# Performance work log

Measured on AMD Instinct MI355X. Metric: run time of the kernel, lower is better.

Reference implementation:

```python
import jax, jax.numpy as jnp
import numpy as np
import math

D_MODEL = 1024
N_HEADS = 16
HEAD_DIM = D_MODEL // N_HEADS  # 64
N_FEATURES = 256
EPS = 1e-06


def _make_orthogonal_features(seed=0):
    # Blocks of QR-orthogonalized gaussian matrices, scaled by sqrt(head_dim)
    rng = np.random.default_rng(seed)
    n_blocks = math.ceil(N_FEATURES / HEAD_DIM)
    blocks = []
    for _ in range(n_blocks):
        q, _ = np.linalg.qr(rng.standard_normal((HEAD_DIM, HEAD_DIM)))
        blocks.append(q)
    mat = np.concatenate(blocks, axis=0)[:N_FEATURES] * math.sqrt(HEAD_DIM)
    return jnp.asarray(mat, dtype=jnp.float32)  # [M, head_dim]


def setup_inputs() -> dict:
    key = jax.random.key(0)
    ks = jax.random.split(key, 6)
    B, L = 4, 4096
    x = jax.random.normal(ks[0], (B, L, D_MODEL), dtype=jnp.float32)

    def lin(k):
        W = jax.random.normal(k, (D_MODEL, D_MODEL), dtype=jnp.float32) * 0.02
        b = jnp.zeros((D_MODEL,), dtype=jnp.float32)
        return W, b

    Wq, bq = lin(ks[1])
    Wk, bk = lin(ks[2])
    Wv, bv = lin(ks[3])
    Wo, bo = lin(ks[4])
    omega = _make_orthogonal_features(0)
    return {"x": x, "Wq": Wq, "bq": bq, "Wk": Wk, "bk": bk,
            "Wv": Wv, "bv": bv, "Wo": Wo, "bo": bo,
            "omega": omega, "causal": 1}


def _phi(x, omega):
    # positive random feature map: exp(omega^T xs - ||xs||^2/2) / sqrt(M)
    xs = x * (HEAD_DIM ** -0.25)                       # [B,H,L,D]
    x_omega = jnp.einsum('bhld,md->bhlm', xs, omega)   # [B,H,L,M]
    x_norm_sq = 0.5 * jnp.sum(xs * xs, axis=-1, keepdims=True)
    return jnp.exp(x_omega - x_norm_sq) / math.sqrt(N_FEATURES)


def _bidirectional(qp, kp, v):
    kv = jnp.einsum('bhlm,bhld->bhmd', kp, v)
    qkv = jnp.einsum('bhlm,bhmd->bhld', qp, kv)
    k_sum = jnp.sum(kp, axis=2)                        # [B,H,M]
    normalizer = jnp.einsum('bhlm,bhm->bhl', qp, k_sum)[..., None] + EPS
    return qkv / normalizer


def _causal(qp, kp, v):
    # prefix-sum recurrence over time via lax.scan
    qs = jnp.moveaxis(qp, 2, 0)   # [L,B,H,M]
    ks = jnp.moveaxis(kp, 2, 0)   # [L,B,H,M]
    vs = jnp.moveaxis(v, 2, 0)    # [L,B,H,D]
    B, H = v.shape[0], v.shape[1]
    kv0 = jnp.zeros((B, H, N_FEATURES, HEAD_DIM), dtype=v.dtype)
    ksum0 = jnp.zeros((B, H, N_FEATURES), dtype=v.dtype)

    def step(carry, inp):
        kv, ksum = carry
        q_t, k_t, v_t = inp
        kv = kv + k_t[..., :, None] * v_t[..., None, :]   # [B,H,M,D]
        ksum = ksum + k_t                                  # [B,H,M]
        num = jnp.einsum('bhm,bhmd->bhd', q_t, kv)
        den = jnp.einsum('bhm,bhm->bh', q_t, ksum)[..., None] + EPS
        return (kv, ksum), num / den

    _, out = jax.lax.scan(step, (kv0, ksum0), (qs, ks, vs))  # out: [L,B,H,D]
    return jnp.moveaxis(out, 0, 2)  # [B,H,L,D]


def reference(x, Wq, bq, Wk, bk, Wv, bv, Wo, bo, omega, causal):
    B, L, _ = x.shape

    def proj(W, b):
        return (x @ W + b).reshape(B, L, N_HEADS, HEAD_DIM).transpose(0, 2, 1, 3)

    q = proj(Wq, bq)
    k = proj(Wk, bk)
    v = proj(Wv, bv)
    qp = _phi(q, omega)
    kp = _phi(k, omega)
    if causal:
        out = _causal(qp, kp, v)
    else:
        out = _bidirectional(qp, kp, v)
    out = out.transpose(0, 2, 1, 3).reshape(B, L, D_MODEL)
    return out @ Wo + bo
```

## Files before the change

kernel.cpp:

```cpp
#include <hip/hip_runtime.h>
#include <hip/hip_bf16.h>


#define B_ 4
#define H_ 16
#define L_ 4096
#define D_ 64
#define M_ 256
#define DM_ 1024
#define BH_ 64
#define NSC 32

typedef unsigned int u32;
typedef unsigned short u16;
typedef __attribute__((ext_vector_type(8))) short bf16x8;
typedef __attribute__((ext_vector_type(4))) float f32x4;

static __device__ __forceinline__ float bf2f(u16 u) {
  return __uint_as_float(((u32)u) << 16);
}
static __device__ __forceinline__ u16 f2bf(float f) {
  u32 x = __float_as_uint(f);
  return (u16)((x + 0x7fffu + ((x >> 16) & 1u)) >> 16);
}
#define MFMA16(a, b, c) __builtin_amdgcn_mfma_f32_16x16x32_bf16((a), (b), (c), 0, 0, 0)

__global__ __launch_bounds__(256) void prep_k(
    const float* __restrict__ x, u16* __restrict__ xb,
    const float* __restrict__ W0, const float* __restrict__ W1,
    const float* __restrict__ W2, const float* __restrict__ W3,
    u16* __restrict__ Wt, const float* __restrict__ om,
    u16* __restrict__ omb) {
  __shared__ u16 tt[64][66];
  const int bid = blockIdx.x, tid = threadIdx.x;
  if (bid < 16384) {
    const int i = bid * 256 + tid;
    float4 f = ((const float4*)x)[i];
    ushort4 u;
    u.x = f2bf(f.x); u.y = f2bf(f.y); u.z = f2bf(f.z); u.w = f2bf(f.w);
    ((ushort4*)xb)[i] = u;
  } else if (bid < 17408) {
    const int rem = bid - 16384;
    const int z = rem >> 8, r2 = rem & 255;
    const int k0 = (r2 >> 4) * 64, n0 = (r2 & 15) * 64;
    const float* W = (z == 0) ? W0 : (z == 1) ? W1 : (z == 2) ? W2 : W3;
    u16* o = Wt + (size_t)z * 1048576ull;
    const int r = tid >> 4, c4 = (tid & 15) << 2;
    for (int rr = r; rr < 64; rr += 16) {
      float4 w4 = *(const float4*)(W + (size_t)(k0 + rr) * DM_ + n0 + c4);
      tt[c4 + 0][rr] = f2bf(w4.x);
      tt[c4 + 1][rr] = f2bf(w4.y);
      tt[c4 + 2][rr] = f2bf(w4.z);
      tt[c4 + 3][rr] = f2bf(w4.w);
    }
    __syncthreads();
    for (int rr = r; rr < 64; rr += 16) {
      ushort4 u4;
      u4.x = tt[rr][c4 + 0];
      u4.y = tt[rr][c4 + 1];
      u4.z = tt[rr][c4 + 2];
      u4.w = tt[rr][c4 + 3];
      *(ushort4*)(o + (size_t)(n0 + rr) * DM_ + k0 + c4) = u4;
    }
  } else {
    const int i = (bid - 17408) * 256 + tid;
    omb[i] = f2bf(om[i] * 0.35355339059327373f);
  }
}

__global__ __launch_bounds__(256) void mm3_k(
    const u16* __restrict__ A, const u16* __restrict__ Wt,
    const float* __restrict__ bq, const float* __restrict__ bk,
    const float* __restrict__ bv, u16* __restrict__ qb,
    u16* __restrict__ kb, u16* __restrict__ vb,
    float* __restrict__ nhq, float* __restrict__ nhk) {
  __shared__ u16 sA[128][64];
  __shared__ u16 sB[128][64];
  const int y = blockIdx.y;
  const u16* Bt = Wt + (size_t)y * 1048576ull;
  const float* bias = (y == 0) ? bq : (y == 1) ? bk : bv;
  u16* outp = (y == 0) ? qb : (y == 1) ? kb : vb;
  float* nhout = (y == 0) ? nhq : (y == 1) ? nhk : nullptr;
  const int tid = threadIdx.x, lane = tid & 63, w = tid >> 6;
  const int fr = lane & 15, fg = lane >> 4;
  const int wr = w >> 1, wc = w & 1;
  const int lb = ((blockIdx.x & 7) << 7) | (blockIdx.x >> 3);
  const int m0 = (lb >> 3) * 128, n0 = (lb & 7) * 128;
  const int srow = tid >> 3, sslot = tid & 7;
  f32x4 acc[4][4] = {};
  bf16x8 av[4], bv4[4];
#pragma unroll
  for (int p = 0; p < 4; ++p) {
    av[p]  = *(const bf16x8*)(A  + (size_t)(m0 + srow + p * 32) * DM_ + sslot * 8);
    bv4[p] = *(const bf16x8*)(Bt + (size_t)(n0 + srow + p * 32) * DM_ + sslot * 8);
  }
  for (int k0 = 0; k0 < DM_; k0 += 64) {
    __syncthreads();
#pragma unroll
    for (int p = 0; p < 4; ++p) {
      const int r = srow + p * 32;
      *(bf16x8*)&sA[r][(sslot ^ (r & 7)) * 8] = av[p];
      *(bf16x8*)&sB[r][(sslot ^ (r & 7)) * 8] = bv4[p];
    }
    if (k0 + 64 < DM_) {
#pragma unroll
      for (int p = 0; p < 4; ++p) {
        av[p]  = *(const bf16x8*)(A  + (size_t)(m0 + srow + p * 32) * DM_ + k0 + 64 + sslot * 8);
        bv4[p] = *(const bf16x8*)(Bt + (size_t)(n0 + srow + p * 32) * DM_ + k0 + 64 + sslot * 8);
      }
    }
    __syncthreads();
#pragma unroll
    for (int ks = 0; ks < 2; ++ks) {
      bf16x8 af[4], bf[4];
#pragma unroll
      for (int i = 0; i < 4; ++i) {
        const int r = wr * 64 + i * 16 + fr;
        af[i] = *(const bf16x8*)&sA[r][((ks * 4 + fg) ^ (r & 7)) * 8];
      }
#pragma unroll
      for (int j = 0; j < 4; ++j) {
        const int r = wc * 64 + j * 16 + fr;
        bf[j] = *(const bf16x8*)&sB[r][((ks * 4 + fg) ^ (r & 7)) * 8];
      }
#pragma unroll
      for (int i = 0; i < 4; ++i)
#pragma unroll
        for (int j = 0; j < 4; ++j)
          acc[i][j] = MFMA16(af[i], bf[j], acc[i][j]);
    }
  }
  const int m_blk = m0 + wr * 64, n_blk = n0 + wc * 64;
  float nhacc[4][4] = {};
#pragma unroll
  for (int j = 0; j < 4; ++j) {
    const int n = n_blk + j * 16 + fr;
    const float bi = bias[n];
    const int h = n >> 6, d = n & 63;
#pragma unroll
    for (int i = 0; i < 4; ++i) {
#pragma unroll
      for (int r = 0; r < 4; ++r) {
        const int m = m_blk + i * 16 + fg * 4 + r;
        const float val = acc[i][j][r] + bi;
        const int b = m >> 12, l = m & 4095;
        const u16 sv = f2bf(val);
        outp[((size_t)(b * H_ + h) * L_ + l) * D_ + d] = sv;
        const float rv = bf2f(sv);
        nhacc[i][r] += rv * rv;
      }
    }
  }
  if (nhout) {
    const int hh2 = n_blk >> 6;
#pragma unroll
    for (int i = 0; i < 4; ++i)
#pragma unroll
      for (int r = 0; r < 4; ++r) {
        float s = nhacc[i][r];
        s += __shfl_xor(s, 1, 64);
        s += __shfl_xor(s, 2, 64);
        s += __shfl_xor(s, 4, 64);
        s += __shfl_xor(s, 8, 64);
        if (fr == 0) {
          const int m = m_blk + i * 16 + fg * 4 + r;
          const int b = m >> 12, l = m & 4095;
          nhout[(size_t)(b * H_ + hh2) * L_ + l] = 0.0625f * s;
        }
      }
  }
}

__global__ __launch_bounds__(256) void mmo_k(
    const u16* __restrict__ A, const u16* __restrict__ Bt,
    const float* __restrict__ bias, float* __restrict__ outp) {
  __shared__ u16 sA[128][64];
  __shared__ u16 sB[128][64];
  const int tid = threadIdx.x, lane = tid & 63, w = tid >> 6;
  const int fr = lane & 15, fg = lane >> 4;
  const int wr = w >> 1, wc = w & 1;
  const int lb = ((blockIdx.x & 7) << 7) | (blockIdx.x >> 3);
  const int m0 = (lb >> 3) * 128, n0 = (lb & 7) * 128;
  const int srow = tid >> 3, sslot = tid & 7;
  f32x4 acc[4][4] = {};
  bf16x8 av[4], bv[4];
#pragma unroll
  for (int p = 0; p < 4; ++p) {
    av[p] = *(const bf16x8*)(A  + (size_t)(m0 + srow + p * 32) * DM_ + sslot * 8);
    bv[p] = *(const bf16x8*)(Bt + (size_t)(n0 + srow + p * 32) * DM_ + sslot * 8);
  }
  for (int k0 = 0; k0 < DM_; k0 += 64) {
    __syncthreads();
#pragma unroll
    for (int p = 0; p < 4; ++p) {
      const int r = srow + p * 32;
      *(bf16x8*)&sA[r][(sslot ^ (r & 7)) * 8] = av[p];
      *(bf16x8*)&sB[r][(sslot ^ (r & 7)) * 8] = bv[p];
    }
    if (k0 + 64 < DM_) {
#pragma unroll
      for (int p = 0; p < 4; ++p) {
        av[p] = *(const bf16x8*)(A  + (size_t)(m0 + srow + p * 32) * DM_ + k0 + 64 + sslot * 8);
        bv[p] = *(const bf16x8*)(Bt + (size_t)(n0 + srow + p * 32) * DM_ + k0 + 64 + sslot * 8);
      }
    }
    __syncthreads();
#pragma unroll
    for (int ks = 0; ks < 2; ++ks) {
      bf16x8 af[4], bf[4];
#pragma unroll
      for (int i = 0; i < 4; ++i) {
        const int r = wr * 64 + i * 16 + fr;
        af[i] = *(const bf16x8*)&sA[r][((ks * 4 + fg) ^ (r & 7)) * 8];
      }
#pragma unroll
      for (int j = 0; j < 4; ++j) {
        const int r = wc * 64 + j * 16 + fr;
        bf[j] = *(const bf16x8*)&sB[r][((ks * 4 + fg) ^ (r & 7)) * 8];
      }
#pragma unroll
      for (int i = 0; i < 4; ++i)
#pragma unroll
        for (int j = 0; j < 4; ++j)
          acc[i][j] = MFMA16(af[i], bf[j], acc[i][j]);
    }
  }
  const int m_blk = m0 + wr * 64, n_blk = n0 + wc * 64;
#pragma unroll
  for (int j = 0; j < 4; ++j) {
    const int n = n_blk + j * 16 + fr;
    const float bi = bias[n];
#pragma unroll
    for (int i = 0; i < 4; ++i)
#pragma unroll
      for (int r = 0; r < 4; ++r) {
        const int m = m_blk + i * 16 + fg * 4 + r;
        outp[(size_t)m * DM_ + n] = acc[i][j][r] + bi;
      }
  }
}

__global__ __launch_bounds__(256) void kvstate_k(
    const u16* __restrict__ k, const u16* __restrict__ v,
    const u16* __restrict__ omb, const float* __restrict__ nhk,
    u16* __restrict__ stateb, float* __restrict__ ksum) {
  __shared__ u16 sPhi[256][72];
  __shared__ u16 sVt[64][72];
  const int tid = threadIdx.x, lane = tid & 63, w = tid >> 6;
  const int fr = lane & 15, fg = lane >> 4;
  const int sc = blockIdx.x, bh = blockIdx.y;
  const size_t base_l = (size_t)bh * L_ + (size_t)sc * 128;

  bf16x8 ones;
#pragma unroll
  for (int e = 0; e < 8; ++e) ones[e] = (short)0x3F80;

  f32x4 kvacc[4][4] = {};
  f32x4 ksacc[4] = {};

  for (int sub = 0; sub < 2; ++sub) {
    const size_t tl = base_l + sub * 64;
    const u16* kg = k + tl * 64;
    __syncthreads();
    {
      const u16* vp = v + (tl + lane) * 64 + w * 16;
      bf16x8 v0 = *(const bf16x8*)(vp);
      bf16x8 v1 = *(const bf16x8*)(vp + 8);
#pragma unroll
      for (int e = 0; e < 8; ++e) sVt[w * 16 + e][lane] = (u16)v0[e];
#pragma unroll
      for (int e = 0; e < 8; ++e) sVt[w * 16 + 8 + e][lane] = (u16)v1[e];
    }
    float nhr[4];
#pragma unroll
    for (int tt = 0; tt < 4; ++tt) nhr[tt] = nhk[tl + tt * 16 + fr];
#pragma unroll
    for (int mi = 0; mi < 4; ++mi) {
      const int m0 = (w << 6) + mi * 16;
      const bf16x8 a0 = *(const bf16x8*)(omb + (m0 + fr) * 64 + fg * 8);
      const bf16x8 a1 = *(const bf16x8*)(omb + (m0 + fr) * 64 + 32 + fg * 8);
#pragma unroll
      for (int tt = 0; tt < 4; ++tt) {
        const bf16x8 b0 = *(const bf16x8*)(kg + (tt * 16 + fr) * 64 + fg * 8);
        const bf16x8 b1 = *(const bf16x8*)(kg + (tt * 16 + fr) * 64 + 32 + fg * 8);
        f32x4 acc = {0.f, 0.f, 0.f, 0.f};
        acc = MFMA16(a0, b0, acc);
        acc = MFMA16(a1, b1, acc);
        const float nhv = nhr[tt];
#pragma unroll
        for (int r = 0; r < 4; ++r)
          sPhi[m0 + fg * 4 + r][tt * 16 + fr] = f2bf(__expf(acc[r] - nhv) * 0.0625f);
      }
    }
    __syncthreads();
#pragma unroll
    for (int mi = 0; mi < 4; ++mi) {
      const int m0 = (w << 6) + mi * 16;
      const bf16x8 pb0 = *(const bf16x8*)&sPhi[m0 + fr][fg * 8];
      const bf16x8 pb1 = *(const bf16x8*)&sPhi[m0 + fr][32 + fg * 8];
      ksacc[mi] = MFMA16(pb0, ones, ksacc[mi]);
      ksacc[mi] = MFMA16(pb1, ones, ksacc[mi]);
#pragma unroll
      for (int dj = 0; dj < 4; ++dj) {
        const bf16x8 va0 = *(const bf16x8*)&sVt[dj * 16 + fr][fg * 8];
        const bf16x8 va1 = *(const bf16x8*)&sVt[dj * 16 + fr][32 + fg * 8];
        kvacc[mi][dj] = MFMA16(va0, pb0, kvacc[mi][dj]);
        kvacc[mi][dj] = MFMA16(va1, pb1, kvacc[mi][dj]);
      }
    }
  }
  u16* stb = stateb + (size_t)(bh * NSC + sc) * (M_ * D_);
  float* ksp = ksum + (size_t)(bh * NSC + sc) * M_;
#pragma unroll
  for (int mi = 0; mi < 4; ++mi) {
    const int m = (w << 6) + mi * 16 + fr;
#pragma unroll
    for (int dj = 0; dj < 4; ++dj)
#pragma unroll
      for (int r = 0; r < 4; ++r)
        stb[(size_t)(dj * 16 + fg * 4 + r) * M_ + m] = f2bf(kvacc[mi][dj][r]);
    if (fr == 0) {
#pragma unroll
      for (int r = 0; r < 4; ++r)
        ksp[(w << 6) + mi * 16 + fg * 4 + r] = ksacc[mi][r];
    }
  }
}

__global__ __launch_bounds__(256) void scan_k(u16* __restrict__ stateb,
                                              float* __restrict__ ksum) {
  const int bh = blockIdx.y;
  u16* sb = stateb + (size_t)bh * NSC * (M_ * D_);
  const int base = blockIdx.x * 2048 + threadIdx.x * 8;
  float run[8] = {};
  for (int cc = 0; cc < NSC; ++cc) {
    u16* st = sb + (size_t)cc * (M_ * D_) + base;
    ushort4 t0 = *(ushort4*)st;
    ushort4 t1 = *(ushort4*)(st + 4);
    ushort4 w0, w1;
    w0.x = f2bf(run[0]); w0.y = f2bf(run[1]); w0.z = f2bf(run[2]); w0.w = f2bf(run[3]);
    w1.x = f2bf(run[4]); w1.y = f2bf(run[5]); w1.z = f2bf(run[6]); w1.w = f2bf(run[7]);
    *(ushort4*)st = w0;
    *(ushort4*)(st + 4) = w1;
    run[0] += bf2f(t0.x); run[1] += bf2f(t0.y); run[2] += bf2f(t0.z); run[3] += bf2f(t0.w);
    run[4] += bf2f(t1.x); run[5] += bf2f(t1.y); run[6] += bf2f(t1.z); run[7] += bf2f(t1.w);
  }
  if (blockIdx.x == 0) {
    float rk = 0.f;
    for (int cc = 0; cc < NSC; ++cc) {
      float* p = ksum + (size_t)(bh * NSC + cc) * M_ + threadIdx.x;
      const float t = *p;
      *p = rk;
      rk += t;
    }
  }
}

static __device__ __forceinline__ void phi_quad(
    const u16* __restrict__ xg, const u16* __restrict__ ombq,
    u16* __restrict__ dst, int dstride, const float* nhv,
    int wb, int lane) {
  const int fr = lane & 15, fg = lane >> 4;
  const int tband = wb * 16;
  const bf16x8 a0 = *(const bf16x8*)(xg + (tband + fr) * 64 + fg * 8);
  const bf16x8 a1 = *(const bf16x8*)(xg + (tband + fr) * 64 + 32 + fg * 8);
#pragma unroll
  for (int j = 0; j < 4; ++j) {
    const bf16x8 b0 = *(const bf16x8*)(ombq + (j * 16 + fr) * 64 + fg * 8);
    const bf16x8 b1 = *(const bf16x8*)(ombq + (j * 16 + fr) * 64 + 32 + fg * 8);
    f32x4 acc = {0.f, 0.f, 0.f, 0.f};
    acc = MFMA16(a0, b0, acc);
    acc = MFMA16(a1, b1, acc);
#pragma unroll
    for (int r = 0; r < 4; ++r) {
      const int t = tband + fg * 4 + r;
      dst[t * dstride + j * 16 + fr] = f2bf(__expf(acc[r] - nhv[r]) * 0.0625f);
    }
  }
}

__global__ __launch_bounds__(512) void outchunk_k(
    const u16* __restrict__ q, const u16* __restrict__ kk,
    const u16* __restrict__ v, const u16* __restrict__ omb,
    const u16* __restrict__ stateb, const float* __restrict__ ksum,
    const float* __restrict__ nhq, const float* __restrict__ nhk,
    u16* __restrict__ attn) {
  __shared__ u16 sKa[64][264];
  __shared__ u16 sKb[64][264];
  __shared__ u16 sS0[64][72];
  __shared__ u16 sS1[64][72];
  __shared__ u16 sB1[64][72];
  __shared__ u16 sB2[64][72];
  __shared__ float ksum_l[256];
  const int tid = threadIdx.x, lane = tid & 63, w = tid >> 6;
  const int h = w >> 2, wl = w & 3;
  const int fr = lane & 15, fg = lane >> 4;
  const int bh = blockIdx.x >> 5, sc = blockIdx.x & 31;
  const size_t base_l = (size_t)bh * L_ + (size_t)sc * 128;
  const size_t tokq = base_l + (size_t)h * 64;
  const u16* qg = q + tokq * 64;
  const u16* stgb = stateb + (size_t)(bh * NSC + sc) * (M_ * D_);
  const float* ksg = ksum + (size_t)(bh * NSC + sc) * M_;

  if (tid < 256) ksum_l[tid] = ksg[tid];

  float nhq4[4];
#pragma unroll
  for (int r = 0; r < 4; ++r) nhq4[r] = nhq[tokq + wl * 16 + fg * 4 + r];

  u16* myscr = (h == 0) ? &sKa[0][0] : &sKb[0][0];
  bf16x8 qa0[2], qa1[2], qa2[2], qa3[2];
  f32x4 oacc[4] = {};
#define QPHASE(MQ, QA)                                                          \
  {                                                                             \
    bf16x8 b0r[4], b1r[4];                                                      \
    _Pragma("unroll")                                                           \
    for (int j = 0; j < 4; ++j) {                                               \
      b0r[j] = *(const bf16x8*)(stgb + (size_t)(j * 16 + fr) * M_ + MQ * 64 + fg * 8);        \
      b1r[j] = *(const bf16x8*)(stgb + (size_t)(j * 16 + fr) * M_ + MQ * 64 + 32 + fg * 8);   \
    }                                                                           \
    phi_quad(qg, omb + MQ * 4096, myscr, 264, nhq4, wl, lane);                  \
    QA[0] = *(const bf16x8*)(myscr + (wl * 16 + fr) * 264 + fg * 8);            \
    QA[1] = *(const bf16x8*)(myscr + (wl * 16 + fr) * 264 + 32 + fg * 8);       \
    __builtin_amdgcn_s_setprio(1);                                              \
    _Pragma("unroll")                                                           \
    for (int j = 0; j < 4; ++j) {                                               \
      oacc[j] = MFMA16(QA[0], b0r[j], oacc[j]);                                 \
      oacc[j] = MFMA16(QA[1], b1r[j], oacc[j]);                                 \
    }                                                                           \
    __builtin_amdgcn_s_setprio(0);                                              \
  }
  QPHASE(0, qa0)
  QPHASE(1, qa1)
  QPHASE(2, qa2)
  QPHASE(3, qa3)
#undef QPHASE
  __syncthreads();

  float denk = 0.f;
#pragma unroll
  for (int e = 0; e < 8; ++e) {
    denk += bf2f((u16)qa0[0][e]) * ksum_l[0   + fg * 8 + e]
          + bf2f((u16)qa0[1][e]) * ksum_l[32  + fg * 8 + e]
          + bf2f((u16)qa1[0][e]) * ksum_l[64  + fg * 8 + e]
          + bf2f((u16)qa1[1][e]) * ksum_l[96  + fg * 8 + e]
          + bf2f((u16)qa2[0][e]) * ksum_l[128 + fg * 8 + e]
          + bf2f((u16)qa2[1][e]) * ksum_l[160 + fg * 8 + e]
          + bf2f((u16)qa3[0][e]) * ksum_l[192 + fg * 8 + e]
          + bf2f((u16)qa3[1][e]) * ksum_l[224 + fg * 8 + e];
  }
  denk += __shfl_xor(denk, 16, 64);
  denk += __shfl_xor(denk, 32, 64);

  {
    const size_t ktokh = base_l + (size_t)h * 64;
    const u16* kgh = kk + ktokh * 64;
    float nhkh[4];
#pragma unroll
    for (int r = 0; r < 4; ++r) nhkh[r] = nhk[ktokh + wl * 16 + fg * 4 + r];
#pragma unroll
    for (int mq = 0; mq < 4; ++mq)
      phi_quad(kgh, omb + mq * 4096, myscr + mq * 64, 264, nhkh, wl, lane);
  }
  bf16x8 v0 = {}, v1 = {}, v2 = {}, v3 = {};
  if (h == 0) {
    const u16* vp0 = v + (base_l + lane) * 64 + wl * 16;
    const u16* vp1 = v + (base_l + 64 + lane) * 64 + wl * 16;
    v0 = *(const bf16x8*)(vp0);
    v1 = *(const bf16x8*)(vp0 + 8);
    v2 = *(const bf16x8*)(vp1);
    v3 = *(const bf16x8*)(vp1 + 8);
  }
  __syncthreads();

  float dS[4] = {0.f, 0.f, 0.f, 0.f};
  {
    f32x4 sacc[4] = {};
    __builtin_amdgcn_s_setprio(1);
#define SPH0(MQ, QA)                                                            \
    _Pragma("unroll")                                                           \
    for (int j = 0; j < 4; ++j) {                                               \
      const bf16x8 b0 = *(const bf16x8*)&sKa[j * 16 + fr][MQ * 64 + fg * 8];    \
      const bf16x8 b1 = *(const bf16x8*)&sKa[j * 16 + fr][MQ * 64 + 32 + fg * 8]; \
      sacc[j] = MFMA16(QA[0], b0, sacc[j]);                                     \
      sacc[j] = MFMA16(QA[1], b1, sacc[j]);                                     \
    }
    SPH0(0, qa0)
    SPH0(1, qa1)
    SPH0(2, qa2)
    SPH0(3, qa3)
#undef SPH0
    __builtin_amdgcn_s_setprio(0);
    u16 (*sSo)[72] = (h == 0) ? sS0 : sS1;
#pragma unroll
    for (int j = 0; j < 4; ++j)
#pragma unroll
      for (int r = 0; r < 4; ++r) {
        const int ss = j * 16 + fr, t = wl * 16 + fg * 4 + r;
        float val = sacc[j][r];
        if (h == 0 && ss > t) val = 0.f;
        const u16 vb = f2bf(val);
        sSo[t][ss] = vb;
        dS[r] += bf2f(vb);
      }
  }
  if (h == 0) {
#pragma unroll
    for (int e = 0; e < 8; ++e) sB1[wl * 16 + e][lane] = (u16)v0[e];
#pragma unroll
    for (int e = 0; e < 8; ++e) sB1[wl * 16 + 8 + e][lane] = (u16)v1[e];
#pragma unroll
    for (int e = 0; e < 8; ++e) sB2[wl * 16 + e][lane] = (u16)v2[e];
#pragma unroll
    for (int e = 0; e < 8; ++e) sB2[wl * 16 + 8 + e][lane] = (u16)v3[e];
  }
  __syncthreads();

  {
    const u16 (*sSo)[72] = (h == 0) ? sS0 : sS1;
    const bf16x8 a0 = *(const bf16x8*)&sSo[wl * 16 + fr][fg * 8];
    const bf16x8 a1 = *(const bf16x8*)&sSo[wl * 16 + fr][32 + fg * 8];
    __builtin_amdgcn_s_setprio(1);
#pragma unroll
    for (int j = 0; j < 4; ++j) {
      const bf16x8 b0 = *(const bf16x8*)&sB1[j * 16 + fr][fg * 8];
      const bf16x8 b1 = *(const bf16x8*)&sB1[j * 16 + fr][32 + fg * 8];
      oacc[j] = MFMA16(a0, b0, oacc[j]);
      oacc[j] = MFMA16(a1, b1, oacc[j]);
    }
    __builtin_amdgcn_s_setprio(0);
  }

  if (h == 1) {
    f32x4 sacc[4] = {};
    __builtin_amdgcn_s_setprio(1);
#define SPH1(MQ, QA)                                                            \
    _Pragma("unroll")                                                           \
    for (int j = 0; j < 4; ++j) {                                               \
      const bf16x8 b0 = *(const bf16x8*)&sKb[j * 16 + fr][MQ * 64 + fg * 8];    \
      const bf16x8 b1 = *(const bf16x8*)&sKb[j * 16 + fr][MQ * 64 + 32 + fg * 8]; \
      sacc[j] = MFMA16(QA[0], b0, sacc[j]);                                     \
      sacc[j] = MFMA16(QA[1], b1, sacc[j]);                                     \
    }
    SPH1(0, qa0)
    SPH1(1, qa1)
    SPH1(2, qa2)
    SPH1(3, qa3)
#undef SPH1
    __builtin_amdgcn_s_setprio(0);
#pragma unroll
    for (int j = 0; j < 4; ++j)
#pragma unroll
      for (int r = 0; r < 4; ++r) {
        const int ss = j * 16 + fr, t = wl * 16 + fg * 4 + r;
        float val = sacc[j][r];
        if (ss > t) val = 0.f;
        const u16 vb = f2bf(val);
        sS1[t][ss] = vb;
        dS[r] += bf2f(vb);
      }
    {
      const bf16x8 a0 = *(const bf16x8*)&sS1[wl * 16 + fr][fg * 8];
      const bf16x8 a1 = *(const bf16x8*)&sS1[wl * 16 + fr][32 + fg * 8];
      __builtin_amdgcn_s_setprio(1);
#pragma unroll
      for (int j = 0; j < 4; ++j) {
        const bf16x8 b0 = *(const bf16x8*)&sB2[j * 16 + fr][fg * 8];
        const bf16x8 b1 = *(const bf16x8*)&sB2[j * 16 + fr][32 + fg * 8];
        oacc[j] = MFMA16(a0, b0, oacc[j]);
        oacc[j] = MFMA16(a1, b1, oacc[j]);
      }
      __builtin_amdgcn_s_setprio(0);
    }
  }

#pragma unroll
  for (int m2 = 1; m2 <= 8; m2 <<= 1) {
#pragma unroll
    for (int r = 0; r < 4; ++r) dS[r] += __shfl_xor(dS[r], m2, 64);
  }
  const int b = bh >> 4, hh = bh & 15;
#pragma unroll
  for (int r = 0; r < 4; ++r) {
    const float dk = __shfl(denk, fg * 4 + r, 64);
    const float rinv = 1.0f / (dk + dS[r] + 1e-6f);
    const int t = wl * 16 + fg * 4 + r;
    const int l = sc * 128 + h * 64 + t;
#pragma unroll
    for (int j = 0; j < 4; ++j) {
      const int d = j * 16 + fr;
      attn[((size_t)b * L_ + l) * DM_ + hh * 64 + d] = f2bf(oacc[j][r] * rinv);
    }
  }
}

extern "C" void kernel_launch(void* const* d_in, const int* in_sizes, int n_in,
                              void* d_out, int out_size, void* d_ws, size_t ws_size,
                              hipStream_t stream) {
  const float* x     = (const float*)d_in[0];
  const float* Wq    = (const float*)d_in[1];
  const float* bq    = (const float*)d_in[2];
  const float* Wk    = (const float*)d_in[3];
  const float* bk    = (const float*)d_in[4];
  const float* Wv    = (const float*)d_in[5];
  const float* bv    = (const float*)d_in[6];
  const float* Wo    = (const float*)d_in[7];
  const float* bo    = (const float*)d_in[8];
  const float* omega = (const float*)d_in[9];
  float* out = (float*)d_out;

  char* ws = (char*)d_ws;
  u16*   v      = (u16*)(ws);
  u16*   qb     = (u16*)(ws + 33554432ull);
  u16*   kb     = (u16*)(ws + 67108864ull);
  u16*   xb     = (u16*)(ws + 100663296ull);
  u16*   attn   = xb;
  u16*   stateb = (u16*)(ws + 134217728ull);
  float* ksum   = (float*)(ws + 201326592ull);
  u16*   Wt     = (u16*)(ws + 203423744ull);
  u16*   omb    = (u16*)(ws + 211812352ull);
  float* nhq    = (float*)(ws + 211845120ull);
  float* nhk    = (float*)(ws + 212893696ull);

  prep_k<<<17472, 256, 0, stream>>>(x, xb, Wq, Wk, Wv, Wo, Wt, omega, omb);
  mm3_k<<<dim3(1024, 3), 256, 0, stream>>>(xb, Wt, bq, bk, bv,
                                           qb, kb, v, nhq, nhk);
  kvstate_k<<<dim3(NSC, BH_), 256, 0, stream>>>(kb, v, omb, nhk, stateb, ksum);
  scan_k<<<dim3(8, BH_), 256, 0, stream>>>(stateb, ksum);
  outchunk_k<<<BH_ * NSC, 512, 0, stream>>>(qb, kb, v, omb, stateb, ksum,
                                            nhq, nhk, attn);
  mmo_k<<<1024, 256, 0, stream>>>(attn, Wt + 3145728ull, bo, out);
}
```

Before: 516.2 us.

## Hoist key feature map before query phase and drop a block barrier

Computes the key feature map into shared memory before the query-phase work and moves the query scratch buffer to the S tiles, so one __syncthreads between the query phase and the S computation can be removed. V loads are split across both halves of the block, with each half transposing 64 tokens instead of one half doing all 128. This reduces barrier stalls and balances the V-transpose work. The query scratch now aliases sS0/sS1, which are later overwritten by S, so correctness depends on barrier ordering that has to be checked.

```diff
diff --git a/kernel.cpp b/kernel.cpp
--- a/kernel.cpp
+++ b/kernel.cpp
@@ -404,11 +404,29 @@
 
   if (tid < 256) ksum_l[tid] = ksg[tid];
 
+  bf16x8 ev0, ev1;
+  {
+    const u16* vp = v + (base_l + (size_t)h * 64 + lane) * 64 + wl * 16;
+    ev0 = *(const bf16x8*)(vp);
+    ev1 = *(const bf16x8*)(vp + 8);
+  }
+
+  u16* kdst = (h == 0) ? &sKa[0][0] : &sKb[0][0];
+  {
+    const size_t ktokh = base_l + (size_t)h * 64;
+    const u16* kgh = kk + ktokh * 64;
+    float nhkh[4];
+#pragma unroll
+    for (int r = 0; r < 4; ++r) nhkh[r] = nhk[ktokh + wl * 16 + fg * 4 + r];
+#pragma unroll
+    for (int mq = 0; mq < 4; ++mq)
+      phi_quad(kgh, omb + mq * 4096, kdst + mq * 64, 264, nhkh, wl, lane);
+  }
+
   float nhq4[4];
 #pragma unroll
   for (int r = 0; r < 4; ++r) nhq4[r] = nhq[tokq + wl * 16 + fg * 4 + r];
-
-  u16* myscr = (h == 0) ? &sKa[0][0] : &sKb[0][0];
+  u16* myscr = (h == 0) ? &sS0[0][0] : &sS1[0][0];
   bf16x8 qa0[2], qa1[2], qa2[2], qa3[2];
   f32x4 oacc[4] = {};
 #define QPHASE(MQ, QA)                                                          \
@@ -419,9 +437,9 @@
       b0r[j] = *(const bf16x8*)(stgb + (size_t)(j * 16 + fr) * M_ + MQ * 64 + fg * 8);        \
       b1r[j] = *(const bf16x8*)(stgb + (size_t)(j * 16 + fr) * M_ + MQ * 64 + 32 + fg * 8);   \
     }                                                                           \
-    phi_quad(qg, omb + MQ * 4096, myscr, 264, nhq4, wl, lane);                  \
-    QA[0] = *(const bf16x8*)(myscr + (wl * 16 + fr) * 264 + fg * 8);            \
-    QA[1] = *(const bf16x8*)(myscr + (wl * 16 + fr) * 264 + 32 + fg * 8);       \
+    phi_quad(qg, omb + MQ * 4096, myscr, 72, nhq4, wl, lane);                   \
+    QA[0] = *(const bf16x8*)(myscr + (wl * 16 + fr) * 72 + fg * 8);             \
+    QA[1] = *(const bf16x8*)(myscr + (wl * 16 + fr) * 72 + 32 + fg * 8);        \
     __builtin_amdgcn_s_setprio(1);                                              \
     _Pragma("unroll")                                                           \
     for (int j = 0; j < 4; ++j) {                                               \
@@ -451,27 +469,6 @@
   }
   denk += __shfl_xor(denk, 16, 64);
   denk += __shfl_xor(denk, 32, 64);
-
-  {
-    const size_t ktokh = base_l + (size_t)h * 64;
-    const u16* kgh = kk + ktokh * 64;
-    float nhkh[4];
-#pragma unroll
-    for (int r = 0; r < 4; ++r) nhkh[r] = nhk[ktokh + wl * 16 + fg * 4 + r];
-#pragma unroll
-    for (int mq = 0; mq < 4; ++mq)
-      phi_quad(kgh, omb + mq * 4096, myscr + mq * 64, 264, nhkh, wl, lane);
-  }
-  bf16x8 v0 = {}, v1 = {}, v2 = {}, v3 = {};
-  if (h == 0) {
-    const u16* vp0 = v + (base_l + lane) * 64 + wl * 16;
-    const u16* vp1 = v + (base_l + 64 + lane) * 64 + wl * 16;
-    v0 = *(const bf16x8*)(vp0);
-    v1 = *(const bf16x8*)(vp0 + 8);
-    v2 = *(const bf16x8*)(vp1);
-    v3 = *(const bf16x8*)(vp1 + 8);
-  }
-  __syncthreads();
 
   float dS[4] = {0.f, 0.f, 0.f, 0.f};
   {
@@ -504,15 +501,12 @@
         dS[r] += bf2f(vb);
       }
   }
-  if (h == 0) {
-#pragma unroll
-    for (int e = 0; e < 8; ++e) sB1[wl * 16 + e][lane] = (u16)v0[e];
-#pragma unroll
-    for (int e = 0; e < 8; ++e) sB1[wl * 16 + 8 + e][lane] = (u16)v1[e];
-#pragma unroll
-    for (int e = 0; e < 8; ++e) sB2[wl * 16 + e][lane] = (u16)v2[e];
-#pragma unroll
-    for (int e = 0; e < 8; ++e) sB2[wl * 16 + 8 + e][lane] = (u16)v3[e];
+  {
+    u16 (*sBo)[72] = (h == 0) ? sB1 : sB2;
+#pragma unroll
+    for (int e = 0; e < 8; ++e) sBo[wl * 16 + e][lane] = (u16)ev0[e];
+#pragma unroll
+    for (int e = 0; e < 8; ++e) sBo[wl * 16 + 8 + e][lane] = (u16)ev1[e];
   }
   __syncthreads();
 
```

New measurement: 505.9 us. 2.0% less time.
